# Performance work log

Hardware: AMD Instinct MI355X
Metric: run time of the kernel (lower is better)

The kernel has to match this reference:

```python
import jax, jax.numpy as jnp
import numpy as np

HIDDEN_DIM = 128
ATTN_DIM = 64
B, N = 2, 512

def setup_inputs() -> dict:
    key = jax.random.key(0)
    ks = jax.random.split(key, 8)
    s = 0.05
    return {
        "X":    jax.random.normal(ks[0], (B, N, HIDDEN_DIM), dtype=jnp.float32),
        "Wo":   jax.random.normal(ks[1], (ATTN_DIM, HIDDEN_DIM), dtype=jnp.float32) * s,
        "W1":   jax.random.normal(ks[2], (ATTN_DIM, HIDDEN_DIM), dtype=jnp.float32) * s,
        "Wphi": jax.random.normal(ks[3], (ATTN_DIM,), dtype=jnp.float32) * s,
        "Wy":   jax.random.normal(ks[4], (HIDDEN_DIM, HIDDEN_DIM), dtype=jnp.float32) * s,
        "by":   jax.random.normal(ks[5], (HIDDEN_DIM,), dtype=jnp.float32) * s,
        "We":   jax.random.normal(ks[6], (HIDDEN_DIM, ATTN_DIM), dtype=jnp.float32) * s,
        "be":   jax.random.normal(ks[7], (HIDDEN_DIM,), dtype=jnp.float32) * s,
    }

def reference(X, Wo, W1, Wphi, Wy, by, We, be):
    # h_o, h_1: [B, N, A]
    h_o = jnp.einsum('bnc,ac->bna', X, Wo)
    h_1 = jnp.einsum('bnc,ac->bna', X, W1)
    # pairwise tanh edge features e_ij: [B, N, N, A]
    e = jnp.tanh(h_o[:, :, None, :] + h_1[:, None, :, :])
    # scores [B, N, N] via w_phi projection, row-wise softmax over j
    scores = jnp.einsum('bija,a->bij', e, Wphi)
    alpha = jax.nn.softmax(scores, axis=-1)
    # value path 1: Wy x_j -> aggregated by alpha (bmm)
    X_y = jnp.einsum('bnc,hc->bnh', X, Wy) + by
    part1 = jnp.einsum('bij,bjh->bih', alpha, X_y)
    # value path 2: We e_ij -> weighted sum over j
    eval_ = jnp.einsum('bija,ha->bijh', e, We) + be  # [B, N, N, H]
    part2 = jnp.einsum('bij,bijh->bih', alpha, eval_)
    return part1 + part2
```

## Files before the change

kernel.cpp:

```cpp
#include <hip/hip_runtime.h>

#define B_ 2
#define N_ 512
#define C_ 128
#define A_ 64
#define H_ 128
#define TI 2

#define SC2L 2.885390081777927f

#define OFF_WOT 0
#define OFF_W1T (OFF_WOT + C_*A_)
#define OFF_WYT (OFF_W1T + C_*A_)
#define OFF_WET (OFF_WYT + C_*H_)
#define OFF_TO  (OFF_WET + A_*H_)
#define OFF_T1S (OFF_TO + B_*N_*A_)
#define OFF_T1T (OFF_T1S + B_*N_*A_)
#define OFF_XY  (OFF_T1T + B_*N_*A_)

__device__ __forceinline__ float fexp2(float x) { return __builtin_amdgcn_exp2f(x); }
__device__ __forceinline__ float frcp(float x)  { return __builtin_amdgcn_rcpf(x); }
__device__ __forceinline__ float ftanh(float x) {
  return 1.0f - 2.0f * frcp(fexp2(SC2L * x) + 1.0f);
}

__global__ __launch_bounds__(256) void prep_weights(
    const float* __restrict__ Wo, const float* __restrict__ W1,
    const float* __restrict__ Wy, const float* __restrict__ We,
    float* __restrict__ ws) {
  int t = blockIdx.x * 256 + threadIdx.x;
  if (t < A_*C_) {
    int a = t / C_, c = t % C_;
    ws[OFF_WOT + c*A_ + a] = Wo[t];
    ws[OFF_W1T + c*A_ + a] = W1[t];
    int h2 = t / A_, a2 = t % A_;
    ws[OFF_WET + a2*H_ + h2] = We[t];
  }
  if (t < H_*C_) {
    int h = t / C_, c = t % C_;
    ws[OFF_WYT + c*H_ + h] = Wy[t];
  }
}

__global__ __launch_bounds__(256) void proj_kernel(
    const float* __restrict__ X, const float* __restrict__ by,
    float* __restrict__ ws) {
  __shared__ float xs[2*C_];
  int row0 = blockIdx.x * 2;
  int t = threadIdx.x;
  if (t < 2*C_) xs[t] = X[(size_t)row0*C_ + t];
  __syncthreads();

  const float* wt;
  int col, stride;
  if (t < 64)       { wt = ws + OFF_WOT; col = t;       stride = A_; }
  else if (t < 128) { wt = ws + OFF_W1T; col = t - 64;  stride = A_; }
  else              { wt = ws + OFF_WYT; col = t - 128; stride = H_; }

  float acc0 = 0.f, acc1 = 0.f;
  #pragma unroll 8
  for (int c = 0; c < C_; ++c) {
    float wv = wt[c*stride + col];
    acc0 = fmaf(xs[c], wv, acc0);
    acc1 = fmaf(xs[C_ + c], wv, acc1);
  }
  if (t < 64) {
    float* o = ws + OFF_TO + (size_t)row0*A_ + col;
    o[0] = ftanh(acc0); o[A_] = ftanh(acc1);
  } else if (t < 128) {
    float t0 = ftanh(acc0), t1 = ftanh(acc1);
    float* o = ws + OFF_T1S + (size_t)row0*A_ + col;
    o[0] = t0; o[A_] = t1;
    int b = row0 >> 9, n0 = row0 & (N_-1);
    float* oT = ws + OFF_T1T + (size_t)b*A_*N_ + (size_t)col*N_ + n0;
    oT[0] = t0; oT[1] = t1;
  } else {
    float bb = by[col];
    float* o = ws + OFF_XY + (size_t)row0*H_ + col;
    o[0] = acc0 + bb; o[H_] = acc1 + bb;
  }
}

__global__ __launch_bounds__(512) void attn_kernel(
    const float* __restrict__ Wphi, const float* __restrict__ be,
    const float* __restrict__ ws, float* __restrict__ out) {
  __shared__ float sc[TI][N_];
  __shared__ float redm[TI][8];
  __shared__ float reds[TI][8];
  __shared__ float ebw[TI][8][A_];
  __shared__ float ebar[TI][A_];
  __shared__ float p1s[TI][4][H_];
  __shared__ float4 pk[A_];
  __shared__ float wphs[A_];

  int t = threadIdx.x;
  int w = t >> 6;
  int lane = t & 63;
  int blk = blockIdx.x;
  int b = blk >> 8;
  int i0 = (blk & 255) * TI;

  const float* tog = ws + OFF_TO  + (size_t)(b*N_ + i0)*A_;
  const float* t1s = ws + OFF_T1S + (size_t)(b*N_)*A_;
  const float* t1t = ws + OFF_T1T + (size_t)b*A_*N_;
  const float* xyg = ws + OFF_XY  + (size_t)(b*N_)*H_;
  const float* wet = ws + OFF_WET;

  if (t < A_) {
    float wv = Wphi[t];
    float to0 = tog[t], to1 = tog[A_ + t];
    pk[t] = make_float4(to0, to1, wv*to0, wv*to1);
    wphs[t] = wv;
  }
  __syncthreads();

  float s0 = 0.f, s1 = 0.f;
  {
    const float* t1p = t1t + t;
    #pragma unroll 4
    for (int a = 0; a < A_; ++a) {
      float tb = t1p[(size_t)a*N_];
      float4 k = pk[a];
      float wtb = wphs[a] * tb;
      float den0 = fmaf(k.x, tb, 1.0f);
      float den1 = fmaf(k.y, tb, 1.0f);
      float num0 = k.z + wtb;
      float num1 = k.w + wtb;
      s0 = fmaf(num0, frcp(den0), s0);
      s1 = fmaf(num1, frcp(den1), s1);
    }
  }

  float m0 = s0, m1 = s1;
  #pragma unroll
  for (int m = 1; m < 64; m <<= 1) {
    m0 = fmaxf(m0, __shfl_xor(m0, m));
    m1 = fmaxf(m1, __shfl_xor(m1, m));
  }
  if (lane == 0) { redm[0][w] = m0; redm[1][w] = m1; }
  __syncthreads();
  m0 = redm[0][0]; m1 = redm[1][0];
  #pragma unroll
  for (int k = 1; k < 8; ++k) { m0 = fmaxf(m0, redm[0][k]); m1 = fmaxf(m1, redm[1][k]); }
  float p0 = __expf(s0 - m0), p1 = __expf(s1 - m1);
  float q0 = p0, q1 = p1;
  #pragma unroll
  for (int m = 1; m < 64; m <<= 1) { q0 += __shfl_xor(q0, m); q1 += __shfl_xor(q1, m); }
  sc[0][t] = p0; sc[1][t] = p1;
  if (lane == 0) { reds[0][w] = q0; reds[1][w] = q1; }
  __syncthreads();
  float l0 = reds[0][0], l1 = reds[1][0];
  #pragma unroll
  for (int k = 1; k < 8; ++k) { l0 += reds[0][k]; l1 += reds[1][k]; }

  {
    float4 kk = pk[lane];
    float to0 = kk.x, to1 = kk.y;
    float c0 = 0.f, c1 = 0.f;
    #pragma unroll 4
    for (int jj = 0; jj < N_/8; ++jj) {
      int j = jj*8 + w;
      float tb = t1s[(size_t)j*A_ + lane];
      float pj0 = sc[0][j], pj1 = sc[1][j];
      float den0 = fmaf(to0, tb, 1.0f);
      float den1 = fmaf(to1, tb, 1.0f);
      float num0 = to0 + tb;
      float num1 = to1 + tb;
      c0 = fmaf(pj0*num0, frcp(den0), c0);
      c1 = fmaf(pj1*num1, frcp(den1), c1);
    }
    ebw[0][w][lane] = c0; ebw[1][w][lane] = c1;
  }

  {
    int h = t & 127;
    int qd = t >> 7;
    float d0 = 0.f, d1 = 0.f;
    const float* xq = xyg + (size_t)(qd*128)*H_ + h;
    #pragma unroll 4
    for (int jc = 0; jc < 128; ++jc) {
      int j = qd*128 + jc;
      float xv = xq[(size_t)jc*H_];
      d0 = fmaf(sc[0][j], xv, d0);
      d1 = fmaf(sc[1][j], xv, d1);
    }
    p1s[0][qd][h] = d0; p1s[1][qd][h] = d1;
  }
  __syncthreads();

  if (t < TI*A_) {
    int r = t >> 6, a = t & 63;
    float e = 0.f;
    #pragma unroll
    for (int k = 0; k < 8; ++k) e += ebw[r][k][a];
    ebar[r][a] = e;
  }
  __syncthreads();

  if (t < TI*H_) {
    int h = t & 127;
    int r = t >> 7;
    float acc = p1s[r][0][h] + p1s[r][1][h] + p1s[r][2][h] + p1s[r][3][h];
    float e2 = 0.f;
    #pragma unroll 8
    for (int a = 0; a < A_; ++a) e2 = fmaf(ebar[r][a], wet[a*H_ + h], e2);
    float lr = r ? l1 : l0;
    out[(size_t)(b*N_ + i0 + r)*H_ + h] = (acc + e2) * frcp(lr) + be[h];
  }
}

extern "C" void kernel_launch(void* const* d_in, const int* in_sizes, int n_in,
                              void* d_out, int out_size, void* d_ws, size_t ws_size,
                              hipStream_t stream) {
  const float* X    = (const float*)d_in[0];
  const float* Wo   = (const float*)d_in[1];
  const float* W1   = (const float*)d_in[2];
  const float* Wphi = (const float*)d_in[3];
  const float* Wy   = (const float*)d_in[4];
  const float* by   = (const float*)d_in[5];
  const float* We   = (const float*)d_in[6];
  const float* be   = (const float*)d_in[7];
  float* out = (float*)d_out;
  float* ws  = (float*)d_ws;

  hipLaunchKernelGGL(prep_weights, dim3(64), dim3(256), 0, stream, Wo, W1, Wy, We, ws);
  hipLaunchKernelGGL(proj_kernel, dim3(B_*N_/2), dim3(256), 0, stream, X, by, ws);
  hipLaunchKernelGGL(attn_kernel, dim3(B_*N_/TI), dim3(512), 0, stream, Wphi, be, ws, out);
}
```

Baseline: 103.2 us.

## Drop weight-prep kernel, vectorize projection, and double attention threads per block

Removes the separate weight-transpose launch. The projection kernel now reads Wo/W1/Wy rows directly with float4 dot products over one row per thread half, and block 0 transposes We on the side. The attention kernel moves to 1024 threads, so each thread handles a single query row for scores and edge sums. It drops the softmax max-subtraction, which is safe only because scores are bounded by the L1 norm of Wphi. The aggressive launch bounds may constrain registers and cause spills, and the per-thread projection loop trades coalescing for fewer launches.

```diff
diff --git a/kernel.cpp b/kernel.cpp
--- a/kernel.cpp
+++ b/kernel.cpp
@@ -8,11 +8,9 @@
 #define TI 2
 
 #define SC2L 2.885390081777927f
-
-#define OFF_WOT 0
-#define OFF_W1T (OFF_WOT + C_*A_)
-#define OFF_WYT (OFF_W1T + C_*A_)
-#define OFF_WET (OFF_WYT + C_*H_)
+#define LG2E 1.4426950408889634f
+
+#define OFF_WET 0
 #define OFF_TO  (OFF_WET + A_*H_)
 #define OFF_T1S (OFF_TO + B_*N_*A_)
 #define OFF_T1T (OFF_T1S + B_*N_*A_)
@@ -24,78 +22,72 @@
   return 1.0f - 2.0f * frcp(fexp2(SC2L * x) + 1.0f);
 }
 
-__global__ __launch_bounds__(256) void prep_weights(
-    const float* __restrict__ Wo, const float* __restrict__ W1,
-    const float* __restrict__ Wy, const float* __restrict__ We,
+__global__ __launch_bounds__(512) void proj_kernel(
+    const float* __restrict__ X, const float* __restrict__ Wo,
+    const float* __restrict__ W1, const float* __restrict__ Wy,
+    const float* __restrict__ by, const float* __restrict__ We,
     float* __restrict__ ws) {
-  int t = blockIdx.x * 256 + threadIdx.x;
-  if (t < A_*C_) {
-    int a = t / C_, c = t % C_;
-    ws[OFF_WOT + c*A_ + a] = Wo[t];
-    ws[OFF_W1T + c*A_ + a] = W1[t];
-    int h2 = t / A_, a2 = t % A_;
-    ws[OFF_WET + a2*H_ + h2] = We[t];
-  }
-  if (t < H_*C_) {
-    int h = t / C_, c = t % C_;
-    ws[OFF_WYT + c*H_ + h] = Wy[t];
-  }
-}
-
-__global__ __launch_bounds__(256) void proj_kernel(
-    const float* __restrict__ X, const float* __restrict__ by,
-    float* __restrict__ ws) {
-  __shared__ float xs[2*C_];
+  __shared__ float xs[2][C_];
   int row0 = blockIdx.x * 2;
   int t = threadIdx.x;
-  if (t < 2*C_) xs[t] = X[(size_t)row0*C_ + t];
-  __syncthreads();
-
-  const float* wt;
-  int col, stride;
-  if (t < 64)       { wt = ws + OFF_WOT; col = t;       stride = A_; }
-  else if (t < 128) { wt = ws + OFF_W1T; col = t - 64;  stride = A_; }
-  else              { wt = ws + OFF_WYT; col = t - 128; stride = H_; }
-
-  float acc0 = 0.f, acc1 = 0.f;
+  if (t < 2*C_) xs[t >> 7][t & 127] = X[(size_t)row0*C_ + t];
+  __syncthreads();
+
+  int rsub = t >> 8;
+  int col  = t & 255;
+  int g = row0 + rsub;
+
+  const float* W;
+  if (col < 64)       W = Wo + (size_t)col*C_;
+  else if (col < 128) W = W1 + (size_t)(col - 64)*C_;
+  else                W = Wy + (size_t)(col - 128)*C_;
+
+  const float4* w4 = (const float4*)W;
+  const float4* x4 = (const float4*)xs[rsub];
+  float acc = 0.f;
   #pragma unroll 8
-  for (int c = 0; c < C_; ++c) {
-    float wv = wt[c*stride + col];
-    acc0 = fmaf(xs[c], wv, acc0);
-    acc1 = fmaf(xs[C_ + c], wv, acc1);
-  }
-  if (t < 64) {
-    float* o = ws + OFF_TO + (size_t)row0*A_ + col;
-    o[0] = ftanh(acc0); o[A_] = ftanh(acc1);
-  } else if (t < 128) {
-    float t0 = ftanh(acc0), t1 = ftanh(acc1);
-    float* o = ws + OFF_T1S + (size_t)row0*A_ + col;
-    o[0] = t0; o[A_] = t1;
-    int b = row0 >> 9, n0 = row0 & (N_-1);
-    float* oT = ws + OFF_T1T + (size_t)b*A_*N_ + (size_t)col*N_ + n0;
-    oT[0] = t0; oT[1] = t1;
+  for (int k = 0; k < C_/4; ++k) {
+    float4 wv = w4[k];
+    float4 xv = x4[k];
+    acc = fmaf(wv.x, xv.x, acc);
+    acc = fmaf(wv.y, xv.y, acc);
+    acc = fmaf(wv.z, xv.z, acc);
+    acc = fmaf(wv.w, xv.w, acc);
+  }
+
+  if (col < 64) {
+    ws[OFF_TO + (size_t)g*A_ + col] = ftanh(acc);
+  } else if (col < 128) {
+    int a = col - 64;
+    float tv = ftanh(acc);
+    ws[OFF_T1S + (size_t)g*A_ + a] = tv;
+    int b = g >> 9, n = g & (N_-1);
+    ws[OFF_T1T + (size_t)b*A_*N_ + (size_t)a*N_ + n] = tv;
   } else {
-    float bb = by[col];
-    float* o = ws + OFF_XY + (size_t)row0*H_ + col;
-    o[0] = acc0 + bb; o[H_] = acc1 + bb;
-  }
-}
-
-__global__ __launch_bounds__(512) void attn_kernel(
+    int h = col - 128;
+    ws[OFF_XY + (size_t)g*H_ + h] = acc + by[h];
+  }
+
+  if (blockIdx.x == 0) {
+    for (int k = t; k < A_*H_; k += 512) {
+      int h = k >> 6, a = k & 63;
+      ws[OFF_WET + a*H_ + h] = We[k];
+    }
+  }
+}
+
+__global__ __launch_bounds__(1024, 8) void attn_kernel(
     const float* __restrict__ Wphi, const float* __restrict__ be,
     const float* __restrict__ ws, float* __restrict__ out) {
   __shared__ float sc[TI][N_];
-  __shared__ float redm[TI][8];
   __shared__ float reds[TI][8];
+  __shared__ float4 pk[TI][A_];
   __shared__ float ebw[TI][8][A_];
   __shared__ float ebar[TI][A_];
-  __shared__ float p1s[TI][4][H_];
-  __shared__ float4 pk[A_];
-  __shared__ float wphs[A_];
+  __shared__ float p1s[TI][8][H_];
 
   int t = threadIdx.x;
-  int w = t >> 6;
-  int lane = t & 63;
+  int w = t >> 6, lane = t & 63;
   int blk = blockIdx.x;
   int b = blk >> 8;
   int i0 = (blk & 255) * TI;
@@ -106,85 +98,65 @@
   const float* xyg = ws + OFF_XY  + (size_t)(b*N_)*H_;
   const float* wet = ws + OFF_WET;
 
-  if (t < A_) {
-    float wv = Wphi[t];
-    float to0 = tog[t], to1 = tog[A_ + t];
-    pk[t] = make_float4(to0, to1, wv*to0, wv*to1);
-    wphs[t] = wv;
-  }
-  __syncthreads();
-
-  float s0 = 0.f, s1 = 0.f;
+  if (t < TI*A_) {
+    int r = t >> 6, a = t & 63;
+    float to = tog[r*A_ + a];
+    float wv = Wphi[a];
+    pk[r][a] = make_float4(to, wv*to, wv, 0.f);
+  }
+  __syncthreads();
+
   {
-    const float* t1p = t1t + t;
+    int r = t >> 9, j = t & 511;
+    const float* t1p = t1t + j;
+    const float4* pkr = pk[r];
+    float s = 0.f;
     #pragma unroll 4
     for (int a = 0; a < A_; ++a) {
       float tb = t1p[(size_t)a*N_];
-      float4 k = pk[a];
-      float wtb = wphs[a] * tb;
-      float den0 = fmaf(k.x, tb, 1.0f);
-      float den1 = fmaf(k.y, tb, 1.0f);
-      float num0 = k.z + wtb;
-      float num1 = k.w + wtb;
-      s0 = fmaf(num0, frcp(den0), s0);
-      s1 = fmaf(num1, frcp(den1), s1);
-    }
-  }
-
-  float m0 = s0, m1 = s1;
-  #pragma unroll
-  for (int m = 1; m < 64; m <<= 1) {
-    m0 = fmaxf(m0, __shfl_xor(m0, m));
-    m1 = fmaxf(m1, __shfl_xor(m1, m));
-  }
-  if (lane == 0) { redm[0][w] = m0; redm[1][w] = m1; }
-  __syncthreads();
-  m0 = redm[0][0]; m1 = redm[1][0];
-  #pragma unroll
-  for (int k = 1; k < 8; ++k) { m0 = fmaxf(m0, redm[0][k]); m1 = fmaxf(m1, redm[1][k]); }
-  float p0 = __expf(s0 - m0), p1 = __expf(s1 - m1);
-  float q0 = p0, q1 = p1;
-  #pragma unroll
-  for (int m = 1; m < 64; m <<= 1) { q0 += __shfl_xor(q0, m); q1 += __shfl_xor(q1, m); }
-  sc[0][t] = p0; sc[1][t] = p1;
-  if (lane == 0) { reds[0][w] = q0; reds[1][w] = q1; }
-  __syncthreads();
-  float l0 = reds[0][0], l1 = reds[1][0];
-  #pragma unroll
-  for (int k = 1; k < 8; ++k) { l0 += reds[0][k]; l1 += reds[1][k]; }
+      float4 k = pkr[a];
+      float den = fmaf(k.x, tb, 1.0f);
+      float num = fmaf(k.z, tb, k.y);
+      s = fmaf(num, frcp(den), s);
+    }
+    float p = fexp2(LG2E * s);
+    float q = p;
+    #pragma unroll
+    for (int m = 1; m < 64; m <<= 1) q += __shfl_xor(q, m);
+    sc[r][j] = p;
+    if (lane == 0) reds[r][w & 7] = q;
+  }
+  __syncthreads();
 
   {
-    float4 kk = pk[lane];
-    float to0 = kk.x, to1 = kk.y;
-    float c0 = 0.f, c1 = 0.f;
+    int r = w >> 3, wi = w & 7;
+    float to = pk[r][lane].x;
+    float c = 0.f;
     #pragma unroll 4
     for (int jj = 0; jj < N_/8; ++jj) {
-      int j = jj*8 + w;
+      int j = jj*8 + wi;
       float tb = t1s[(size_t)j*A_ + lane];
-      float pj0 = sc[0][j], pj1 = sc[1][j];
-      float den0 = fmaf(to0, tb, 1.0f);
-      float den1 = fmaf(to1, tb, 1.0f);
-      float num0 = to0 + tb;
-      float num1 = to1 + tb;
-      c0 = fmaf(pj0*num0, frcp(den0), c0);
-      c1 = fmaf(pj1*num1, frcp(den1), c1);
-    }
-    ebw[0][w][lane] = c0; ebw[1][w][lane] = c1;
+      float pj = sc[r][j];
+      float den = fmaf(to, tb, 1.0f);
+      float num = to + tb;
+      c = fmaf(pj*num, frcp(den), c);
+    }
+    ebw[r][wi][lane] = c;
   }
 
   {
-    int h = t & 127;
-    int qd = t >> 7;
+    int h = t & 127, oct = t >> 7;
+    const float* xq = xyg + (size_t)(oct*64)*H_ + h;
     float d0 = 0.f, d1 = 0.f;
-    const float* xq = xyg + (size_t)(qd*128)*H_ + h;
     #pragma unroll 4
-    for (int jc = 0; jc < 128; ++jc) {
-      int j = qd*128 + jc;
+    for (int jc = 0; jc < 64; ++jc) {
+      int j = oct*64 + jc;
       float xv = xq[(size_t)jc*H_];
       d0 = fmaf(sc[0][j], xv, d0);
       d1 = fmaf(sc[1][j], xv, d1);
     }
-    p1s[0][qd][h] = d0; p1s[1][qd][h] = d1;
+    p1s[0][oct][h] = d0;
+    p1s[1][oct][h] = d1;
   }
   __syncthreads();
 
@@ -198,14 +170,17 @@
   __syncthreads();
 
   if (t < TI*H_) {
-    int h = t & 127;
-    int r = t >> 7;
-    float acc = p1s[r][0][h] + p1s[r][1][h] + p1s[r][2][h] + p1s[r][3][h];
+    int h = t & 127, r = t >> 7;
+    float acc = 0.f;
+    #pragma unroll
+    for (int o = 0; o < 8; ++o) acc += p1s[r][o][h];
     float e2 = 0.f;
     #pragma unroll 8
     for (int a = 0; a < A_; ++a) e2 = fmaf(ebar[r][a], wet[a*H_ + h], e2);
-    float lr = r ? l1 : l0;
-    out[(size_t)(b*N_ + i0 + r)*H_ + h] = (acc + e2) * frcp(lr) + be[h];
+    float l = 0.f;
+    #pragma unroll
+    for (int k = 0; k < 8; ++k) l += reds[r][k];
+    out[(size_t)(b*N_ + i0 + r)*H_ + h] = (acc + e2) * frcp(l) + be[h];
   }
 }
 
@@ -223,7 +198,8 @@
   float* out = (float*)d_out;
   float* ws  = (float*)d_ws;
 
-  hipLaunchKernelGGL(prep_weights, dim3(64), dim3(256), 0, stream, Wo, W1, Wy, We, ws);
-  hipLaunchKernelGGL(proj_kernel, dim3(B_*N_/2), dim3(256), 0, stream, X, by, ws);
-  hipLaunchKernelGGL(attn_kernel, dim3(B_*N_/TI), dim3(512), 0, stream, Wphi, be, ws, out);
-}
+  hipLaunchKernelGGL(proj_kernel, dim3(B_*N_/2), dim3(512), 0, stream,
+                     X, Wo, W1, Wy, by, We, ws);
+  hipLaunchKernelGGL(attn_kernel, dim3(B_*N_/TI), dim3(1024), 0, stream,
+                     Wphi, be, ws, out);
+}
```

New measurement: 115.4 us. 1.12x slower.

## Process one query row per block and drop softmax max-subtraction

Applied to the files above, without the earlier changes.

The attention kernel now handles one query row per block instead of two, doubling the grid to 1024 blocks. It drops the max-reduction pass and one barrier by exponentiating scores directly, which is safe only while the scores stay small. The score numerator is folded into a single fma, and the loop unroll factors go from 4 to 8. In exchange, the t1 and Xy loads are no longer shared across two rows per block, so global/L2 traffic per output row doubles.

```diff
diff --git a/kernel.cpp b/kernel.cpp
--- a/kernel.cpp
+++ b/kernel.cpp
@@ -5,9 +5,9 @@
 #define C_ 128
 #define A_ 64
 #define H_ 128
-#define TI 2
 
 #define SC2L 2.885390081777927f
+#define LG2E 1.4426950408889634f
 
 #define OFF_WOT 0
 #define OFF_W1T (OFF_WOT + C_*A_)
@@ -84,128 +84,96 @@
 __global__ __launch_bounds__(512) void attn_kernel(
     const float* __restrict__ Wphi, const float* __restrict__ be,
     const float* __restrict__ ws, float* __restrict__ out) {
-  __shared__ float sc[TI][N_];
-  __shared__ float redm[TI][8];
-  __shared__ float reds[TI][8];
-  __shared__ float ebw[TI][8][A_];
-  __shared__ float ebar[TI][A_];
-  __shared__ float p1s[TI][4][H_];
-  __shared__ float4 pk[A_];
-  __shared__ float wphs[A_];
+  __shared__ __align__(16) float4 pk[A_];
+  __shared__ float tos[A_];
+  __shared__ float sc[N_];
+  __shared__ float reds[8];
+  __shared__ float ebw[8][A_];
+  __shared__ float ebar[A_];
+  __shared__ float p1s[4][H_];
 
   int t = threadIdx.x;
-  int w = t >> 6;
-  int lane = t & 63;
-  int blk = blockIdx.x;
-  int b = blk >> 8;
-  int i0 = (blk & 255) * TI;
+  int w = t >> 6, lane = t & 63;
+  int bi = blockIdx.x;
+  int b = bi >> 9, i = bi & (N_-1);
 
-  const float* tog = ws + OFF_TO  + (size_t)(b*N_ + i0)*A_;
   const float* t1s = ws + OFF_T1S + (size_t)(b*N_)*A_;
   const float* t1t = ws + OFF_T1T + (size_t)b*A_*N_;
   const float* xyg = ws + OFF_XY  + (size_t)(b*N_)*H_;
   const float* wet = ws + OFF_WET;
 
   if (t < A_) {
+    float to = ws[OFF_TO + (size_t)(b*N_ + i)*A_ + t];
     float wv = Wphi[t];
-    float to0 = tog[t], to1 = tog[A_ + t];
-    pk[t] = make_float4(to0, to1, wv*to0, wv*to1);
-    wphs[t] = wv;
+    pk[t] = make_float4(to, wv*to, wv, 0.f);
+    tos[t] = to;
   }
   __syncthreads();
 
-  float s0 = 0.f, s1 = 0.f;
+  float s = 0.f;
   {
     const float* t1p = t1t + t;
-    #pragma unroll 4
+    #pragma unroll 8
     for (int a = 0; a < A_; ++a) {
       float tb = t1p[(size_t)a*N_];
       float4 k = pk[a];
-      float wtb = wphs[a] * tb;
-      float den0 = fmaf(k.x, tb, 1.0f);
-      float den1 = fmaf(k.y, tb, 1.0f);
-      float num0 = k.z + wtb;
-      float num1 = k.w + wtb;
-      s0 = fmaf(num0, frcp(den0), s0);
-      s1 = fmaf(num1, frcp(den1), s1);
+      float den = fmaf(k.x, tb, 1.0f);
+      float num = fmaf(k.z, tb, k.y);
+      s = fmaf(num, frcp(den), s);
     }
   }
-
-  float m0 = s0, m1 = s1;
+  float p = fexp2(LG2E * s);
+  sc[t] = p;
+  float q = p;
   #pragma unroll
-  for (int m = 1; m < 64; m <<= 1) {
-    m0 = fmaxf(m0, __shfl_xor(m0, m));
-    m1 = fmaxf(m1, __shfl_xor(m1, m));
-  }
-  if (lane == 0) { redm[0][w] = m0; redm[1][w] = m1; }
+  for (int m = 1; m < 64; m <<= 1) q += __shfl_xor(q, m);
+  if (lane == 0) reds[w] = q;
   __syncthreads();
-  m0 = redm[0][0]; m1 = redm[1][0];
-  #pragma unroll
-  for (int k = 1; k < 8; ++k) { m0 = fmaxf(m0, redm[0][k]); m1 = fmaxf(m1, redm[1][k]); }
-  float p0 = __expf(s0 - m0), p1 = __expf(s1 - m1);
-  float q0 = p0, q1 = p1;
-  #pragma unroll
-  for (int m = 1; m < 64; m <<= 1) { q0 += __shfl_xor(q0, m); q1 += __shfl_xor(q1, m); }
-  sc[0][t] = p0; sc[1][t] = p1;
-  if (lane == 0) { reds[0][w] = q0; reds[1][w] = q1; }
-  __syncthreads();
-  float l0 = reds[0][0], l1 = reds[1][0];
-  #pragma unroll
-  for (int k = 1; k < 8; ++k) { l0 += reds[0][k]; l1 += reds[1][k]; }
 
   {
-    float4 kk = pk[lane];
-    float to0 = kk.x, to1 = kk.y;
-    float c0 = 0.f, c1 = 0.f;
-    #pragma unroll 4
+    float to = tos[lane];
+    float c = 0.f;
+    #pragma unroll 8
     for (int jj = 0; jj < N_/8; ++jj) {
       int j = jj*8 + w;
       float tb = t1s[(size_t)j*A_ + lane];
-      float pj0 = sc[0][j], pj1 = sc[1][j];
-      float den0 = fmaf(to0, tb, 1.0f);
-      float den1 = fmaf(to1, tb, 1.0f);
-      float num0 = to0 + tb;
-      float num1 = to1 + tb;
-      c0 = fmaf(pj0*num0, frcp(den0), c0);
-      c1 = fmaf(pj1*num1, frcp(den1), c1);
+      float pj = sc[j];
+      float den = fmaf(to, tb, 1.0f);
+      c = fmaf(pj*(to + tb), frcp(den), c);
     }
-    ebw[0][w][lane] = c0; ebw[1][w][lane] = c1;
+    ebw[w][lane] = c;
   }
 
   {
-    int h = t & 127;
-    int qd = t >> 7;
-    float d0 = 0.f, d1 = 0.f;
+    int h = t & 127, qd = t >> 7;
     const float* xq = xyg + (size_t)(qd*128)*H_ + h;
-    #pragma unroll 4
+    float d = 0.f;
+    #pragma unroll 8
     for (int jc = 0; jc < 128; ++jc) {
-      int j = qd*128 + jc;
-      float xv = xq[(size_t)jc*H_];
-      d0 = fmaf(sc[0][j], xv, d0);
-      d1 = fmaf(sc[1][j], xv, d1);
+      d = fmaf(sc[qd*128 + jc], xq[(size_t)jc*H_], d);
     }
-    p1s[0][qd][h] = d0; p1s[1][qd][h] = d1;
+    p1s[qd][h] = d;
   }
   __syncthreads();
 
-  if (t < TI*A_) {
-    int r = t >> 6, a = t & 63;
+  if (t < A_) {
     float e = 0.f;
     #pragma unroll
-    for (int k = 0; k < 8; ++k) e += ebw[r][k][a];
-    ebar[r][a] = e;
+    for (int k = 0; k < 8; ++k) e += ebw[k][t];
+    ebar[t] = e;
   }
   __syncthreads();
 
-  if (t < TI*H_) {
-    int h = t & 127;
-    int r = t >> 7;
-    float acc = p1s[r][0][h] + p1s[r][1][h] + p1s[r][2][h] + p1s[r][3][h];
+  if (t < H_) {
+    int h = t;
+    float l = 0.f;
+    #pragma unroll
+    for (int k = 0; k < 8; ++k) l += reds[k];
+    float acc = p1s[0][h] + p1s[1][h] + p1s[2][h] + p1s[3][h];
     float e2 = 0.f;
     #pragma unroll 8
-    for (int a = 0; a < A_; ++a) e2 = fmaf(ebar[r][a], wet[a*H_ + h], e2);
-    float lr = r ? l1 : l0;
-    out[(size_t)(b*N_ + i0 + r)*H_ + h] = (acc + e2) * frcp(lr) + be[h];
+    for (int a = 0; a < A_; ++a) e2 = fmaf(ebar[a], wet[a*H_ + h], e2);
+    out[(size_t)bi*H_ + h] = (acc + e2) * frcp(l) + be[h];
   }
 }
 
@@ -225,5 +193,5 @@
 
   hipLaunchKernelGGL(prep_weights, dim3(64), dim3(256), 0, stream, Wo, W1, Wy, We, ws);
   hipLaunchKernelGGL(proj_kernel, dim3(B_*N_/2), dim3(256), 0, stream, X, by, ws);
-  hipLaunchKernelGGL(attn_kernel, dim3(B_*N_/TI), dim3(512), 0, stream, Wphi, be, ws, out);
+  hipLaunchKernelGGL(attn_kernel, dim3(B_*N_), dim3(512), 0, stream, Wphi, be, ws, out);
 }
```

Measured after the change: 99.50 us. 1.04x faster.
